# Performance work log

Measured on AMD Instinct MI355X. Metric: run time of the kernel, lower is better.

The kernel has to match this reference:

```python
import jax, jax.numpy as jnp
import numpy as np

B, S, H = 1024, 512, 768
D1, D2 = 128, 1


def setup_inputs() -> dict:
    key = jax.random.key(0)
    k_feat, k_start, k_len, k_w1, k_w2 = jax.random.split(key, 5)
    features_extract = jax.random.normal(k_feat, (B, S, H), dtype=jnp.float32)
    start_token_idx = jax.random.randint(k_start, (B,), 1, 200, dtype=jnp.int64)
    span_len = jax.random.randint(k_len, (B,), 1, 65, dtype=jnp.int64)
    end_token_idx = start_token_idx + span_len  # guaranteed start < end <= 264 < S
    W1 = jax.random.normal(k_w1, (2 * H, D1), dtype=jnp.float32) * (1.0 / np.sqrt(2 * H))
    b1 = jnp.zeros((D1,), dtype=jnp.float32)
    W2 = jax.random.normal(k_w2, (D1, D2), dtype=jnp.float32) * (1.0 / np.sqrt(D1))
    b2 = jnp.zeros((D2,), dtype=jnp.float32)
    return {
        "features_extract": features_extract,
        "start_token_idx": start_token_idx,
        "end_token_idx": end_token_idx,
        "W1": W1, "b1": b1, "W2": W2, "b2": b2,
    }


def reference(features_extract, start_token_idx, end_token_idx, W1, b1, W2, b2):
    # CLS feature: token 0 of each example -> [B, 1, H]
    features_cls = features_extract[:, 0, :][:, None, :]

    # Ragged span mean-pool (vectorized replacement for the per-example loop):
    # mask[b, s] = start[b] <= s < end[b]
    pos = jnp.arange(features_extract.shape[1])  # [S]
    mask = (pos[None, :] >= start_token_idx[:, None]) & (pos[None, :] < end_token_idx[:, None])
    maskf = mask.astype(features_extract.dtype)  # [B, S]
    span_sum = jnp.einsum('bsh,bs->bh', features_extract, maskf)
    span_len = (end_token_idx - start_token_idx).astype(features_extract.dtype)  # >= 1
    features_crc = (span_sum / span_len[:, None])[:, None, :]  # [B, 1, H]

    # Concat + MLP head (dropout layers are identity in eval)
    features = jnp.concatenate([features_cls, features_crc], axis=2)  # [B, 1, 2H]
    h = jax.nn.relu(jnp.einsum('bid,dk->bik', features, W1) + b1)
    out = jax.nn.sigmoid(jnp.einsum('bik,ko->bio', h, W2) + b2)  # [B, 1, 1]
    return out
```

## Files before the change

kernel.cpp:

```cpp
#include <hip/hip_runtime.h>
#include <math.h>

constexpr int Bn = 1024;
constexpr int S  = 512;
constexpr int H  = 768;
constexpr int D1 = 128;
constexpr int HV = H / 4;
constexpr int NH = 512;


__device__ __forceinline__ void head_inner(
    const float (*g)[384], float (*part)[4][D1], const float* __restrict__ W1,
    float* __restrict__ P, int dglob0, int c, int e0, int t) {
  const int k = t & (D1 - 1);
  const int sub = t >> 7;
  const int gofs = sub * 192;
  const float* Wc = W1 + (size_t)(dglob0 + gofs) * D1 + k;

  float a0 = 0.f, a1 = 0.f, a2 = 0.f, a3 = 0.f;
  #pragma unroll 4
  for (int d = 0; d < 192; d += 4) {
    float w0 = Wc[(size_t)(d + 0) * D1];
    float w1 = Wc[(size_t)(d + 1) * D1];
    float w2 = Wc[(size_t)(d + 2) * D1];
    float w3 = Wc[(size_t)(d + 3) * D1];
    float4 g0 = *reinterpret_cast<const float4*>(&g[0][gofs + d]);
    float4 g1 = *reinterpret_cast<const float4*>(&g[1][gofs + d]);
    float4 g2 = *reinterpret_cast<const float4*>(&g[2][gofs + d]);
    float4 g3 = *reinterpret_cast<const float4*>(&g[3][gofs + d]);
    a0 += g0.x * w0 + g0.y * w1 + g0.z * w2 + g0.w * w3;
    a1 += g1.x * w0 + g1.y * w1 + g1.z * w2 + g1.w * w3;
    a2 += g2.x * w0 + g2.y * w1 + g2.z * w2 + g2.w * w3;
    a3 += g3.x * w0 + g3.y * w1 + g3.z * w2 + g3.w * w3;
  }
  part[sub][0][k] = a0;
  part[sub][1][k] = a1;
  part[sub][2][k] = a2;
  part[sub][3][k] = a3;
  __syncthreads();

  if (t < D1) {
    #pragma unroll
    for (int e = 0; e < 4; ++e) {
      P[((size_t)c * Bn + (e0 + e)) * D1 + t] = part[0][e][t] + part[1][e][t];
    }
  }
}

__global__ __launch_bounds__(256) void fused_pool_clshead(
    const float* __restrict__ feat, const int* __restrict__ start,
    const int* __restrict__ endp, float* __restrict__ gp,
    const float* __restrict__ W1, float* __restrict__ P) {
  __shared__ float g[4][384];
  __shared__ float part[2][4][D1];

  const int t = threadIdx.x;

  if (blockIdx.x < NH) {
    const int c = blockIdx.x & 1;
    const int e0 = (blockIdx.x >> 1) * 4;
    const int dglob0 = c * 384;

    for (int i = t; i < 384; i += 256) {
      const int e = i / 96;
      const int j = i % 96;
      float4 v = *reinterpret_cast<const float4*>(
          feat + (size_t)(e0 + e) * S * H + dglob0 + j * 4);
      reinterpret_cast<float4*>(&g[e][0])[j] = v;
    }
    __syncthreads();
    head_inner(g, part, W1, P, dglob0, c, e0, t);
    return;
  }

  if (t >= 192) return;
  const int bb = blockIdx.x - NH;
  const int b = bb >> 1;
  const int p = bb & 1;
  const float4* base = reinterpret_cast<const float4*>(feat) + (size_t)b * (S * HV);

  const int s0 = start[b];
  const int s1 = endp[b];
  float4 a0{0,0,0,0}, a1{0,0,0,0}, a2{0,0,0,0}, a3{0,0,0,0};
  int s = s0 + p;
  for (; s + 6 < s1; s += 8) {
    float4 v0 = base[(size_t)(s    ) * HV + t];
    float4 v1 = base[(size_t)(s + 2) * HV + t];
    float4 v2 = base[(size_t)(s + 4) * HV + t];
    float4 v3 = base[(size_t)(s + 6) * HV + t];
    a0.x += v0.x; a0.y += v0.y; a0.z += v0.z; a0.w += v0.w;
    a1.x += v1.x; a1.y += v1.y; a1.z += v1.z; a1.w += v1.w;
    a2.x += v2.x; a2.y += v2.y; a2.z += v2.z; a2.w += v2.w;
    a3.x += v3.x; a3.y += v3.y; a3.z += v3.z; a3.w += v3.w;
  }
  for (; s < s1; s += 2) {
    float4 v = base[(size_t)s * HV + t];
    a0.x += v.x; a0.y += v.y; a0.z += v.z; a0.w += v.w;
  }
  const float inv = 1.0f / (float)(s1 - s0);
  float4 r;
  r.x = ((a0.x + a1.x) + (a2.x + a3.x)) * inv;
  r.y = ((a0.y + a1.y) + (a2.y + a3.y)) * inv;
  r.z = ((a0.z + a1.z) + (a2.z + a3.z)) * inv;
  r.w = ((a0.w + a1.w) + (a2.w + a3.w)) * inv;
  reinterpret_cast<float4*>(gp)[((size_t)p * Bn + b) * HV + t] = r;
}

__global__ __launch_bounds__(256) void crc_head(
    const float* __restrict__ gp, const float* __restrict__ W1,
    float* __restrict__ P) {
  __shared__ float g[4][384];
  __shared__ float part[2][4][D1];

  const int t = threadIdx.x;
  const int c = 2 + (blockIdx.x & 1);
  const int e0 = (blockIdx.x >> 1) * 4;
  const int dglob0 = c * 384;
  const int dd0 = dglob0 - H;

  for (int i = t; i < 384; i += 256) {
    const int e = i / 96;
    const int j = i % 96;
    const float* b0 = gp + (size_t)(e0 + e) * H + dd0;
    float4 u0 = reinterpret_cast<const float4*>(b0)[j];
    float4 u1 = reinterpret_cast<const float4*>(b0 + (size_t)Bn * H)[j];
    float4 v;
    v.x = u0.x + u1.x; v.y = u0.y + u1.y;
    v.z = u0.z + u1.z; v.w = u0.w + u1.w;
    reinterpret_cast<float4*>(&g[e][0])[j] = v;
  }
  __syncthreads();
  head_inner(g, part, W1, P, dglob0, c, e0, t);
}

__global__ __launch_bounds__(256) void finalize(
    const float* __restrict__ P, const float* __restrict__ b1,
    const float* __restrict__ W2, const float* __restrict__ b2,
    float* __restrict__ out) {
  const int t = threadIdx.x;
  const int w = t >> 6, l = t & 63;
  const int e = blockIdx.x * 4 + w;
  const int k0 = l, k1 = l + 64;
  float h0 = b1[k0], h1 = b1[k1];
  #pragma unroll
  for (int c = 0; c < 4; ++c) {
    h0 += P[((size_t)c * Bn + e) * D1 + k0];
    h1 += P[((size_t)c * Bn + e) * D1 + k1];
  }
  h0 = fmaxf(h0, 0.f); h1 = fmaxf(h1, 0.f);
  float v = h0 * W2[k0] + h1 * W2[k1];
  #pragma unroll
  for (int off = 32; off > 0; off >>= 1) v += __shfl_down(v, off);
  if (l == 0) out[e] = 1.0f / (1.0f + expf(-(v + b2[0])));
}

extern "C" void kernel_launch(void* const* d_in, const int* in_sizes, int n_in,
                              void* d_out, int out_size, void* d_ws, size_t ws_size,
                              hipStream_t stream) {
  const float* feat = (const float*)d_in[0];
  const int* start  = (const int*)d_in[1];
  const int* endp   = (const int*)d_in[2];
  const float* W1   = (const float*)d_in[3];
  const float* b1   = (const float*)d_in[4];
  const float* W2   = (const float*)d_in[5];
  const float* b2   = (const float*)d_in[6];
  float* out = (float*)d_out;

  float* wsf = (float*)d_ws;
  float* gp  = wsf;
  float* P   = gp + (size_t)2 * Bn * H;

  hipLaunchKernelGGL(fused_pool_clshead, dim3(NH + Bn * 2), dim3(256), 0,
                     stream, feat, start, endp, gp, W1, P);
  hipLaunchKernelGGL(crc_head, dim3(NH), dim3(256), 0, stream, gp, W1, P);
  hipLaunchKernelGGL(finalize, dim3(Bn / 4), dim3(256), 0, stream,
                     P, b1, W2, b2, out);
}
```

Before: 34.54 us.

## Fuse CRC head with finalize and schedule pooling blocks before CLS head

Merges the crc_head and finalize kernels into one kernel: each block handles two examples over the full 768-wide CRC half of W1, then adds the CLS partials, applies bias, ReLU, the W2 dot product and the sigmoid in place. This removes one kernel launch and the round trip of CRC partials through global memory. It also reorders block indices so the long-running span-pooling blocks come first and the CLS head blocks last, which should balance the tail. The cost is that W1 is re-read per pair of examples instead of per group of four, which adds W1 traffic.

Result: slower. 41.97 us (+21.5%).

```diff
diff --git a/kernel.cpp b/kernel.cpp
--- a/kernel.cpp
+++ b/kernel.cpp
@@ -6,46 +6,8 @@
 constexpr int H  = 768;
 constexpr int D1 = 128;
 constexpr int HV = H / 4;
-constexpr int NH = 512;
+constexpr int NPOOL = Bn * 2;
 
-
-__device__ __forceinline__ void head_inner(
-    const float (*g)[384], float (*part)[4][D1], const float* __restrict__ W1,
-    float* __restrict__ P, int dglob0, int c, int e0, int t) {
-  const int k = t & (D1 - 1);
-  const int sub = t >> 7;
-  const int gofs = sub * 192;
-  const float* Wc = W1 + (size_t)(dglob0 + gofs) * D1 + k;
-
-  float a0 = 0.f, a1 = 0.f, a2 = 0.f, a3 = 0.f;
-  #pragma unroll 4
-  for (int d = 0; d < 192; d += 4) {
-    float w0 = Wc[(size_t)(d + 0) * D1];
-    float w1 = Wc[(size_t)(d + 1) * D1];
-    float w2 = Wc[(size_t)(d + 2) * D1];
-    float w3 = Wc[(size_t)(d + 3) * D1];
-    float4 g0 = *reinterpret_cast<const float4*>(&g[0][gofs + d]);
-    float4 g1 = *reinterpret_cast<const float4*>(&g[1][gofs + d]);
-    float4 g2 = *reinterpret_cast<const float4*>(&g[2][gofs + d]);
-    float4 g3 = *reinterpret_cast<const float4*>(&g[3][gofs + d]);
-    a0 += g0.x * w0 + g0.y * w1 + g0.z * w2 + g0.w * w3;
-    a1 += g1.x * w0 + g1.y * w1 + g1.z * w2 + g1.w * w3;
-    a2 += g2.x * w0 + g2.y * w1 + g2.z * w2 + g2.w * w3;
-    a3 += g3.x * w0 + g3.y * w1 + g3.z * w2 + g3.w * w3;
-  }
-  part[sub][0][k] = a0;
-  part[sub][1][k] = a1;
-  part[sub][2][k] = a2;
-  part[sub][3][k] = a3;
-  __syncthreads();
-
-  if (t < D1) {
-    #pragma unroll
-    for (int e = 0; e < 4; ++e) {
-      P[((size_t)c * Bn + (e0 + e)) * D1 + t] = part[0][e][t] + part[1][e][t];
-    }
-  }
-}
 
 __global__ __launch_bounds__(256) void fused_pool_clshead(
     const float* __restrict__ feat, const int* __restrict__ start,
@@ -56,9 +18,10 @@
 
   const int t = threadIdx.x;
 
-  if (blockIdx.x < NH) {
-    const int c = blockIdx.x & 1;
-    const int e0 = (blockIdx.x >> 1) * 4;
+  if (blockIdx.x >= NPOOL) {
+    const int hb = blockIdx.x - NPOOL;
+    const int c = hb & 1;
+    const int e0 = (hb >> 1) * 4;
     const int dglob0 = c * 384;
 
     for (int i = t; i < 384; i += 256) {
@@ -69,12 +32,45 @@
       reinterpret_cast<float4*>(&g[e][0])[j] = v;
     }
     __syncthreads();
-    head_inner(g, part, W1, P, dglob0, c, e0, t);
+
+    const int k = t & (D1 - 1);
+    const int sub = t >> 7;
+    const int gofs = sub * 192;
+    const float* Wc = W1 + (size_t)(dglob0 + gofs) * D1 + k;
+
+    float a0 = 0.f, a1 = 0.f, a2 = 0.f, a3 = 0.f;
+    #pragma unroll 4
+    for (int d = 0; d < 192; d += 4) {
+      float w0 = Wc[(size_t)(d + 0) * D1];
+      float w1 = Wc[(size_t)(d + 1) * D1];
+      float w2 = Wc[(size_t)(d + 2) * D1];
+      float w3 = Wc[(size_t)(d + 3) * D1];
+      float4 g0 = *reinterpret_cast<const float4*>(&g[0][gofs + d]);
+      float4 g1 = *reinterpret_cast<const float4*>(&g[1][gofs + d]);
+      float4 g2 = *reinterpret_cast<const float4*>(&g[2][gofs + d]);
+      float4 g3 = *reinterpret_cast<const float4*>(&g[3][gofs + d]);
+      a0 += g0.x * w0 + g0.y * w1 + g0.z * w2 + g0.w * w3;
+      a1 += g1.x * w0 + g1.y * w1 + g1.z * w2 + g1.w * w3;
+      a2 += g2.x * w0 + g2.y * w1 + g2.z * w2 + g2.w * w3;
+      a3 += g3.x * w0 + g3.y * w1 + g3.z * w2 + g3.w * w3;
+    }
+    part[sub][0][k] = a0;
+    part[sub][1][k] = a1;
+    part[sub][2][k] = a2;
+    part[sub][3][k] = a3;
+    __syncthreads();
+
+    if (t < D1) {
+      #pragma unroll
+      for (int e = 0; e < 4; ++e) {
+        P[((size_t)c * Bn + (e0 + e)) * D1 + t] = part[0][e][t] + part[1][e][t];
+      }
+    }
     return;
   }
 
   if (t >= 192) return;
-  const int bb = blockIdx.x - NH;
+  const int bb = blockIdx.x;
   const int b = bb >> 1;
   const int p = bb & 1;
   const float4* base = reinterpret_cast<const float4*>(feat) + (size_t)b * (S * HV);
@@ -106,22 +102,22 @@
   reinterpret_cast<float4*>(gp)[((size_t)p * Bn + b) * HV + t] = r;
 }
 
-__global__ __launch_bounds__(256) void crc_head(
+__global__ __launch_bounds__(256) void crc_head_finalize(
     const float* __restrict__ gp, const float* __restrict__ W1,
-    float* __restrict__ P) {
-  __shared__ float g[4][384];
-  __shared__ float part[2][4][D1];
+    const float* __restrict__ P, const float* __restrict__ b1,
+    const float* __restrict__ W2, const float* __restrict__ b2,
+    float* __restrict__ out) {
+  __shared__ float g[2][768];
+  __shared__ float part[2][2][D1];
+  __shared__ float wsum[4];
 
   const int t = threadIdx.x;
-  const int c = 2 + (blockIdx.x & 1);
-  const int e0 = (blockIdx.x >> 1) * 4;
-  const int dglob0 = c * 384;
-  const int dd0 = dglob0 - H;
+  const int e0 = blockIdx.x * 2;
 
   for (int i = t; i < 384; i += 256) {
-    const int e = i / 96;
-    const int j = i % 96;
-    const float* b0 = gp + (size_t)(e0 + e) * H + dd0;
+    const int e = i / 192;
+    const int j = i % 192;
+    const float* b0 = gp + (size_t)(e0 + e) * H;
     float4 u0 = reinterpret_cast<const float4*>(b0)[j];
     float4 u1 = reinterpret_cast<const float4*>(b0 + (size_t)Bn * H)[j];
     float4 v;
@@ -130,28 +126,46 @@
     reinterpret_cast<float4*>(&g[e][0])[j] = v;
   }
   __syncthreads();
-  head_inner(g, part, W1, P, dglob0, c, e0, t);
-}
 
-__global__ __launch_bounds__(256) void finalize(
-    const float* __restrict__ P, const float* __restrict__ b1,
-    const float* __restrict__ W2, const float* __restrict__ b2,
-    float* __restrict__ out) {
-  const int t = threadIdx.x;
-  const int w = t >> 6, l = t & 63;
-  const int e = blockIdx.x * 4 + w;
-  const int k0 = l, k1 = l + 64;
-  float h0 = b1[k0], h1 = b1[k1];
-  #pragma unroll
-  for (int c = 0; c < 4; ++c) {
-    h0 += P[((size_t)c * Bn + e) * D1 + k0];
-    h1 += P[((size_t)c * Bn + e) * D1 + k1];
+  const int k = t & (D1 - 1);
+  const int sub = t >> 7;
+  const int gofs = sub * 384;
+  const float* Wc = W1 + (size_t)(H + gofs) * D1 + k;
+
+  float a0 = 0.f, a1 = 0.f;
+  #pragma unroll 4
+  for (int d = 0; d < 384; d += 4) {
+    float w0 = Wc[(size_t)(d + 0) * D1];
+    float w1 = Wc[(size_t)(d + 1) * D1];
+    float w2 = Wc[(size_t)(d + 2) * D1];
+    float w3 = Wc[(size_t)(d + 3) * D1];
+    float4 g0 = *reinterpret_cast<const float4*>(&g[0][gofs + d]);
+    float4 g1 = *reinterpret_cast<const float4*>(&g[1][gofs + d]);
+    a0 += g0.x * w0 + g0.y * w1 + g0.z * w2 + g0.w * w3;
+    a1 += g1.x * w0 + g1.y * w1 + g1.z * w2 + g1.w * w3;
   }
-  h0 = fmaxf(h0, 0.f); h1 = fmaxf(h1, 0.f);
-  float v = h0 * W2[k0] + h1 * W2[k1];
-  #pragma unroll
-  for (int off = 32; off > 0; off >>= 1) v += __shfl_down(v, off);
-  if (l == 0) out[e] = 1.0f / (1.0f + expf(-(v + b2[0])));
+  part[sub][0][k] = a0;
+  part[sub][1][k] = a1;
+  __syncthreads();
+
+  {
+    const int e = t >> 7;
+    const int kk = t & (D1 - 1);
+    float h = b1[kk] + part[0][e][kk] + part[1][e][kk]
+            + P[((size_t)0 * Bn + (e0 + e)) * D1 + kk]
+            + P[((size_t)1 * Bn + (e0 + e)) * D1 + kk];
+    h = fmaxf(h, 0.f);
+    float v = h * W2[kk];
+    #pragma unroll
+    for (int off = 32; off > 0; off >>= 1) v += __shfl_down(v, off);
+    if ((t & 63) == 0) wsum[t >> 6] = v;
+  }
+  __syncthreads();
+
+  if (t < 2) {
+    float s = wsum[2 * t] + wsum[2 * t + 1] + b2[0];
+    out[e0 + t] = 1.0f / (1.0f + expf(-s));
+  }
 }
 
 extern "C" void kernel_launch(void* const* d_in, const int* in_sizes, int n_in,
@@ -170,9 +184,8 @@
   float* gp  = wsf;
   float* P   = gp + (size_t)2 * Bn * H;
 
-  hipLaunchKernelGGL(fused_pool_clshead, dim3(NH + Bn * 2), dim3(256), 0,
+  hipLaunchKernelGGL(fused_pool_clshead, dim3(NPOOL + 512), dim3(256), 0,
                      stream, feat, start, endp, gp, W1, P);
-  hipLaunchKernelGGL(crc_head, dim3(NH), dim3(256), 0, stream, gp, W1, P);
-  hipLaunchKernelGGL(finalize, dim3(Bn / 4), dim3(256), 0, stream,
-                     P, b1, W2, b2, out);
+  hipLaunchKernelGGL(crc_head_finalize, dim3(Bn / 2), dim3(256), 0, stream,
+                     gp, W1, P, b1, W2, b2, out);
 }
```

## Fuse span pooling with CRC head GEMV into one block per example

Applied to the files above, without the earlier changes.

Each pooling block now handles one example end to end. It sums the whole span, keeps the mean in shared memory and multiplies it directly against the second half of W1 to write a per-example partial. This removes the gp workspace round trip and the separate crc_head launch, and also drops the two-way split of each span. The cost is half as many pooling blocks, fewer independent loads in flight per example, and an extra W1 read of 768x128 per example rather than per group of four. A min-blocks launch bound of 6 is added.

New measurement: 37.99 us. 1.1x slower.

```diff
diff --git a/kernel.cpp b/kernel.cpp
--- a/kernel.cpp
+++ b/kernel.cpp
@@ -6,59 +6,24 @@
 constexpr int H  = 768;
 constexpr int D1 = 128;
 constexpr int HV = H / 4;
-constexpr int NH = 512;
+constexpr int NCLS = 512;
 
 
-__device__ __forceinline__ void head_inner(
-    const float (*g)[384], float (*part)[4][D1], const float* __restrict__ W1,
-    float* __restrict__ P, int dglob0, int c, int e0, int t) {
-  const int k = t & (D1 - 1);
-  const int sub = t >> 7;
-  const int gofs = sub * 192;
-  const float* Wc = W1 + (size_t)(dglob0 + gofs) * D1 + k;
-
-  float a0 = 0.f, a1 = 0.f, a2 = 0.f, a3 = 0.f;
-  #pragma unroll 4
-  for (int d = 0; d < 192; d += 4) {
-    float w0 = Wc[(size_t)(d + 0) * D1];
-    float w1 = Wc[(size_t)(d + 1) * D1];
-    float w2 = Wc[(size_t)(d + 2) * D1];
-    float w3 = Wc[(size_t)(d + 3) * D1];
-    float4 g0 = *reinterpret_cast<const float4*>(&g[0][gofs + d]);
-    float4 g1 = *reinterpret_cast<const float4*>(&g[1][gofs + d]);
-    float4 g2 = *reinterpret_cast<const float4*>(&g[2][gofs + d]);
-    float4 g3 = *reinterpret_cast<const float4*>(&g[3][gofs + d]);
-    a0 += g0.x * w0 + g0.y * w1 + g0.z * w2 + g0.w * w3;
-    a1 += g1.x * w0 + g1.y * w1 + g1.z * w2 + g1.w * w3;
-    a2 += g2.x * w0 + g2.y * w1 + g2.z * w2 + g2.w * w3;
-    a3 += g3.x * w0 + g3.y * w1 + g3.z * w2 + g3.w * w3;
-  }
-  part[sub][0][k] = a0;
-  part[sub][1][k] = a1;
-  part[sub][2][k] = a2;
-  part[sub][3][k] = a3;
-  __syncthreads();
-
-  if (t < D1) {
-    #pragma unroll
-    for (int e = 0; e < 4; ++e) {
-      P[((size_t)c * Bn + (e0 + e)) * D1 + t] = part[0][e][t] + part[1][e][t];
-    }
-  }
-}
-
-__global__ __launch_bounds__(256) void fused_pool_clshead(
+__global__ __launch_bounds__(256, 6) void fused_launch1(
     const float* __restrict__ feat, const int* __restrict__ start,
-    const int* __restrict__ endp, float* __restrict__ gp,
-    const float* __restrict__ W1, float* __restrict__ P) {
+    const int* __restrict__ endp, const float* __restrict__ W1,
+    float* __restrict__ P, float* __restrict__ Pcrc) {
   __shared__ float g[4][384];
   __shared__ float part[2][4][D1];
+  __shared__ float gcrc[H];
+  __shared__ float pcrc[2][D1];
 
   const int t = threadIdx.x;
+  const unsigned bid = blockIdx.x;
 
-  if (blockIdx.x < NH) {
-    const int c = blockIdx.x & 1;
-    const int e0 = (blockIdx.x >> 1) * 4;
+  if (bid < NCLS) {
+    const int c = bid & 1;
+    const int e0 = (bid >> 1) * 4;
     const int dglob0 = c * 384;
 
     for (int i = t; i < 384; i += 256) {
@@ -69,84 +34,117 @@
       reinterpret_cast<float4*>(&g[e][0])[j] = v;
     }
     __syncthreads();
-    head_inner(g, part, W1, P, dglob0, c, e0, t);
+
+    const int k = t & (D1 - 1);
+    const int sub = t >> 7;
+    const int gofs = sub * 192;
+    const float* Wc = W1 + (size_t)(dglob0 + gofs) * D1 + k;
+
+    float a0 = 0.f, a1 = 0.f, a2 = 0.f, a3 = 0.f;
+    #pragma unroll 4
+    for (int d = 0; d < 192; d += 4) {
+      float w0 = Wc[(size_t)(d + 0) * D1];
+      float w1 = Wc[(size_t)(d + 1) * D1];
+      float w2 = Wc[(size_t)(d + 2) * D1];
+      float w3 = Wc[(size_t)(d + 3) * D1];
+      float4 g0 = *reinterpret_cast<const float4*>(&g[0][gofs + d]);
+      float4 g1 = *reinterpret_cast<const float4*>(&g[1][gofs + d]);
+      float4 g2 = *reinterpret_cast<const float4*>(&g[2][gofs + d]);
+      float4 g3 = *reinterpret_cast<const float4*>(&g[3][gofs + d]);
+      a0 += g0.x * w0 + g0.y * w1 + g0.z * w2 + g0.w * w3;
+      a1 += g1.x * w0 + g1.y * w1 + g1.z * w2 + g1.w * w3;
+      a2 += g2.x * w0 + g2.y * w1 + g2.z * w2 + g2.w * w3;
+      a3 += g3.x * w0 + g3.y * w1 + g3.z * w2 + g3.w * w3;
+    }
+    part[sub][0][k] = a0;
+    part[sub][1][k] = a1;
+    part[sub][2][k] = a2;
+    part[sub][3][k] = a3;
+    __syncthreads();
+
+    if (t < D1) {
+      #pragma unroll
+      for (int e = 0; e < 4; ++e) {
+        P[((size_t)c * Bn + (e0 + e)) * D1 + t] = part[0][e][t] + part[1][e][t];
+      }
+    }
     return;
   }
 
-  if (t >= 192) return;
-  const int bb = blockIdx.x - NH;
-  const int b = bb >> 1;
-  const int p = bb & 1;
-  const float4* base = reinterpret_cast<const float4*>(feat) + (size_t)b * (S * HV);
-
-  const int s0 = start[b];
-  const int s1 = endp[b];
-  float4 a0{0,0,0,0}, a1{0,0,0,0}, a2{0,0,0,0}, a3{0,0,0,0};
-  int s = s0 + p;
-  for (; s + 6 < s1; s += 8) {
-    float4 v0 = base[(size_t)(s    ) * HV + t];
-    float4 v1 = base[(size_t)(s + 2) * HV + t];
-    float4 v2 = base[(size_t)(s + 4) * HV + t];
-    float4 v3 = base[(size_t)(s + 6) * HV + t];
-    a0.x += v0.x; a0.y += v0.y; a0.z += v0.z; a0.w += v0.w;
-    a1.x += v1.x; a1.y += v1.y; a1.z += v1.z; a1.w += v1.w;
-    a2.x += v2.x; a2.y += v2.y; a2.z += v2.z; a2.w += v2.w;
-    a3.x += v3.x; a3.y += v3.y; a3.z += v3.z; a3.w += v3.w;
-  }
-  for (; s < s1; s += 2) {
-    float4 v = base[(size_t)s * HV + t];
-    a0.x += v.x; a0.y += v.y; a0.z += v.z; a0.w += v.w;
-  }
-  const float inv = 1.0f / (float)(s1 - s0);
-  float4 r;
-  r.x = ((a0.x + a1.x) + (a2.x + a3.x)) * inv;
-  r.y = ((a0.y + a1.y) + (a2.y + a3.y)) * inv;
-  r.z = ((a0.z + a1.z) + (a2.z + a3.z)) * inv;
-  r.w = ((a0.w + a1.w) + (a2.w + a3.w)) * inv;
-  reinterpret_cast<float4*>(gp)[((size_t)p * Bn + b) * HV + t] = r;
-}
-
-__global__ __launch_bounds__(256) void crc_head(
-    const float* __restrict__ gp, const float* __restrict__ W1,
-    float* __restrict__ P) {
-  __shared__ float g[4][384];
-  __shared__ float part[2][4][D1];
-
-  const int t = threadIdx.x;
-  const int c = 2 + (blockIdx.x & 1);
-  const int e0 = (blockIdx.x >> 1) * 4;
-  const int dglob0 = c * 384;
-  const int dd0 = dglob0 - H;
-
-  for (int i = t; i < 384; i += 256) {
-    const int e = i / 96;
-    const int j = i % 96;
-    const float* b0 = gp + (size_t)(e0 + e) * H + dd0;
-    float4 u0 = reinterpret_cast<const float4*>(b0)[j];
-    float4 u1 = reinterpret_cast<const float4*>(b0 + (size_t)Bn * H)[j];
-    float4 v;
-    v.x = u0.x + u1.x; v.y = u0.y + u1.y;
-    v.z = u0.z + u1.z; v.w = u0.w + u1.w;
-    reinterpret_cast<float4*>(&g[e][0])[j] = v;
+  const int b = bid - NCLS;
+  if (t < 192) {
+    const float4* base =
+        reinterpret_cast<const float4*>(feat) + (size_t)b * (S * HV);
+    const int s0 = start[b];
+    const int s1 = endp[b];
+    float4 a0{0,0,0,0}, a1{0,0,0,0}, a2{0,0,0,0}, a3{0,0,0,0};
+    int s = s0;
+    for (; s + 3 < s1; s += 4) {
+      float4 v0 = base[(size_t)(s + 0) * HV + t];
+      float4 v1 = base[(size_t)(s + 1) * HV + t];
+      float4 v2 = base[(size_t)(s + 2) * HV + t];
+      float4 v3 = base[(size_t)(s + 3) * HV + t];
+      a0.x += v0.x; a0.y += v0.y; a0.z += v0.z; a0.w += v0.w;
+      a1.x += v1.x; a1.y += v1.y; a1.z += v1.z; a1.w += v1.w;
+      a2.x += v2.x; a2.y += v2.y; a2.z += v2.z; a2.w += v2.w;
+      a3.x += v3.x; a3.y += v3.y; a3.z += v3.z; a3.w += v3.w;
+    }
+    for (; s < s1; ++s) {
+      float4 v = base[(size_t)s * HV + t];
+      a0.x += v.x; a0.y += v.y; a0.z += v.z; a0.w += v.w;
+    }
+    const float inv = 1.0f / (float)(s1 - s0);
+    float4 r;
+    r.x = ((a0.x + a1.x) + (a2.x + a3.x)) * inv;
+    r.y = ((a0.y + a1.y) + (a2.y + a3.y)) * inv;
+    r.z = ((a0.z + a1.z) + (a2.z + a3.z)) * inv;
+    r.w = ((a0.w + a1.w) + (a2.w + a3.w)) * inv;
+    reinterpret_cast<float4*>(gcrc)[t] = r;
   }
   __syncthreads();
-  head_inner(g, part, W1, P, dglob0, c, e0, t);
+
+  {
+    const int k = t & (D1 - 1);
+    const int sub = t >> 7;
+    const float* Wc = W1 + (size_t)(H + sub * 384) * D1 + k;
+    const float* gb = gcrc + sub * 384;
+    float accA = 0.f, accB = 0.f;
+    #pragma unroll 4
+    for (int j = 0; j < 384; j += 8) {
+      float w0 = Wc[(size_t)(j + 0) * D1];
+      float w1 = Wc[(size_t)(j + 1) * D1];
+      float w2 = Wc[(size_t)(j + 2) * D1];
+      float w3 = Wc[(size_t)(j + 3) * D1];
+      float w4 = Wc[(size_t)(j + 4) * D1];
+      float w5 = Wc[(size_t)(j + 5) * D1];
+      float w6 = Wc[(size_t)(j + 6) * D1];
+      float w7 = Wc[(size_t)(j + 7) * D1];
+      float4 gA = *reinterpret_cast<const float4*>(gb + j);
+      float4 gB = *reinterpret_cast<const float4*>(gb + j + 4);
+      accA += gA.x * w0 + gA.y * w1 + gA.z * w2 + gA.w * w3;
+      accB += gB.x * w4 + gB.y * w5 + gB.z * w6 + gB.w * w7;
+    }
+    pcrc[sub][k] = accA + accB;
+  }
+  __syncthreads();
+
+  if (t < D1) {
+    Pcrc[(size_t)b * D1 + t] = pcrc[0][t] + pcrc[1][t];
+  }
 }
 
 __global__ __launch_bounds__(256) void finalize(
-    const float* __restrict__ P, const float* __restrict__ b1,
-    const float* __restrict__ W2, const float* __restrict__ b2,
-    float* __restrict__ out) {
+    const float* __restrict__ P, const float* __restrict__ Pcrc,
+    const float* __restrict__ b1, const float* __restrict__ W2,
+    const float* __restrict__ b2, float* __restrict__ out) {
   const int t = threadIdx.x;
   const int w = t >> 6, l = t & 63;
   const int e = blockIdx.x * 4 + w;
   const int k0 = l, k1 = l + 64;
-  float h0 = b1[k0], h1 = b1[k1];
-  #pragma unroll
-  for (int c = 0; c < 4; ++c) {
-    h0 += P[((size_t)c * Bn + e) * D1 + k0];
-    h1 += P[((size_t)c * Bn + e) * D1 + k1];
-  }
+  float h0 = b1[k0] + P[((size_t)0 * Bn + e) * D1 + k0]
+           + P[((size_t)1 * Bn + e) * D1 + k0] + Pcrc[(size_t)e * D1 + k0];
+  float h1 = b1[k1] + P[((size_t)0 * Bn + e) * D1 + k1]
+           + P[((size_t)1 * Bn + e) * D1 + k1] + Pcrc[(size_t)e * D1 + k1];
   h0 = fmaxf(h0, 0.f); h1 = fmaxf(h1, 0.f);
   float v = h0 * W2[k0] + h1 * W2[k1];
   #pragma unroll
@@ -166,13 +164,12 @@
   const float* b2   = (const float*)d_in[6];
   float* out = (float*)d_out;
 
-  float* wsf = (float*)d_ws;
-  float* gp  = wsf;
-  float* P   = gp + (size_t)2 * Bn * H;
+  float* wsf  = (float*)d_ws;
+  float* P    = wsf;
+  float* Pcrc = P + (size_t)2 * Bn * D1;
 
-  hipLaunchKernelGGL(fused_pool_clshead, dim3(NH + Bn * 2), dim3(256), 0,
-                     stream, feat, start, endp, gp, W1, P);
-  hipLaunchKernelGGL(crc_head, dim3(NH), dim3(256), 0, stream, gp, W1, P);
+  hipLaunchKernelGGL(fused_launch1, dim3(NCLS + Bn), dim3(256), 0, stream,
+                     feat, start, endp, W1, P, Pcrc);
   hipLaunchKernelGGL(finalize, dim3(Bn / 4), dim3(256), 0, stream,
-                     P, b1, W2, b2, out);
+                     P, Pcrc, b1, W2, b2, out);
 }
```
